# Kernel optimization log

Hardware: AMD Instinct MI355X
Metric: run time of the kernel (lower is better)

Reference implementation:

```python
import jax, jax.numpy as jnp
import numpy as np

EPS = 1e-10
LN_EPS = 1e-5
NEG = -1e30
H = 8  # attention_head


def _layernorm(x, g, b):
    mu = jnp.mean(x, axis=-1, keepdims=True)
    var = jnp.mean(jnp.square(x - mu), axis=-1, keepdims=True)
    return (x - mu) * jax.lax.rsqrt(var + LN_EPS) * g + b


def setup_inputs() -> dict:
    key = jax.random.key(0)
    ks = jax.random.split(key, 10)
    B, T, D = 4, 1024, 1024
    inputs = jax.random.normal(ks[0], (B, T, D), dtype=jnp.float32)
    lengths = jax.random.randint(ks[1], (B,), T // 2, T + 1).astype(jnp.int32)
    lengths = lengths.at[0].set(T)  # at least one full-length sequence
    noise_u = jax.random.uniform(ks[2], (B, H, T, T), dtype=jnp.float32)
    w = lambda k: (jax.random.normal(k, (D, D), dtype=jnp.float32) * 0.02)
    return {
        'inputs': inputs, 'lengths': lengths, 'noise_u': noise_u,
        'Wq': w(ks[3]), 'Wk': w(ks[4]), 'Wv': w(ks[5]),
        'Weq': w(ks[6]), 'Wek': w(ks[7]), 'Wfc': w(ks[8]),
        'bfc': jnp.zeros((D,), jnp.float32),
        'ln1_g': jnp.ones((D,), jnp.float32), 'ln1_b': jnp.zeros((D,), jnp.float32),
        'ln2_g': jnp.ones((D,), jnp.float32), 'ln2_b': jnp.zeros((D,), jnp.float32),
    }


def reference(inputs, lengths, noise_u, Wq, Wk, Wv, Weq, Wek, Wfc, bfc,
              ln1_g, ln1_b, ln2_g, ln2_b):
    B, T, D = inputs.shape
    dh = D // H
    # length mask: True where padded
    pad = jnp.arange(T)[None, :] >= lengths[:, None]            # (B, T)
    x = jnp.where(pad[:, :, None], 0.0, inputs)                  # zero padded positions

    def heads(W):
        h = x @ W.T                                              # (B,T,D)
        return h.reshape(B, T, H, dh).transpose(0, 2, 1, 3)      # (B,H,T,dh)

    q, k, v, eq, ek = (heads(W) for W in (Wq, Wk, Wv, Weq, Wek))
    scores = jnp.einsum('bhqd,bhkd->bhqk', q, k) / jnp.sqrt(jnp.float32(D))
    edge = jnp.einsum('bhqd,bhkd->bhqk', eq, ek)                 # (B,H,T,T)

    # bernoulli prior: binary-concrete sample (hard threshold), tau=1
    edges_prob = jax.nn.sigmoid(edge)
    logistic = jnp.log(noise_u + EPS) - jnp.log(1.0 - noise_u + EPS)
    y_soft = jax.nn.sigmoid(jnp.log(edges_prob + EPS) - jnp.log(1.0 - edges_prob + EPS) + logistic)
    gate = y_soft > 0.5                                          # hard edges (condition only, as in torch .data)

    valid = gate & (~pad[:, None, None, :])                      # gate AND key-length mask
    s = jnp.where(valid, scores, NEG)
    attn = jax.nn.softmax(s, axis=-1)
    attn = jnp.where(jnp.any(valid, axis=-1, keepdims=True), attn, 0.0)  # nan->0 for fully-masked rows

    ctx = jax.nn.relu(jnp.einsum('bhqk,bhkd->bhqd', attn, v))
    ctx = ctx.transpose(0, 2, 1, 3).reshape(B, T, D)

    h1 = _layernorm(ctx + x, ln1_g, ln1_b)
    h2 = jax.nn.relu(h1 @ Wfc.T + bfc) + h1
    out = _layernorm(h2, ln2_g, ln2_b)
    out = jnp.where(pad[:, :, None], 0.0, out)
    return out, attn, edges_prob
```

## Files before the change

### kernel.cpp

```cpp
#include <hip/hip_runtime.h>
#include <math.h>

constexpr int Bn = 4, Tn = 1024, Dn = 1024, Hn = 8, DH = 128;
constexpr float EPSF = 1e-10f;
constexpr float LN_EPSF = 1e-5f;
constexpr float NEGF = -1e30f;

typedef __attribute__((ext_vector_type(8))) short bf16x8;
typedef __attribute__((ext_vector_type(4))) float f32x4;
typedef __attribute__((ext_vector_type(4))) unsigned uint4v;

#define MFMA16(a, b, c) __builtin_amdgcn_mfma_f32_16x16x32_bf16(a, b, c, 0, 0, 0)

__device__ __forceinline__ short f2bf(float f) {
    unsigned u = __builtin_bit_cast(unsigned, f);
    u += 0x7fffu + ((u >> 16) & 1u);
    return (short)(u >> 16);
}
__device__ __forceinline__ float bf2f(short h) {
    return __builtin_bit_cast(float, ((unsigned)(unsigned short)h) << 16);
}
__device__ __forceinline__ unsigned pack2(float a, float b) {
    return ((unsigned)(unsigned short)f2bf(a)) | (((unsigned)(unsigned short)f2bf(b)) << 16);
}

__device__ __forceinline__ void gload16(const void* g, void* l) {
    __builtin_amdgcn_global_load_lds((__attribute__((address_space(1))) void*)g,
                                     (__attribute__((address_space(3))) void*)l,
                                     16, 0, 0);
}

template <int NW>
__device__ __forceinline__ void stage_b(const short* g, int ld, short* lds, int lane, int wid) {
#pragma unroll
    for (int s = 0; s < 8 / NW; ++s) {
        const int ii = wid * (8 / NW) + s;
        const int c = ii * 64 + lane;
        const int kb = c >> 7, r = c & 127;
        gload16(g + (size_t)r * ld + kb * 8, lds + ii * 512);
    }
}

template <int NT>
__device__ __forceinline__ void stage64(const short* g, int ld, short* lds, int lane, int wid) {
    constexpr int IT = 1024 / NT;
#pragma unroll
    for (int s = 0; s < IT; ++s) {
        const int cb = wid * IT + s;
        const int c = cb * 64 + lane;
        const int kb = c >> 7, r = c & 127;
        gload16(g + (size_t)r * ld + kb * 8, lds + cb * 512);
    }
}

template <int NW>
__device__ __forceinline__ void stage_f(const float* g, int ld, float* lds, int lane, int wid) {
#pragma unroll
    for (int s = 0; s < 16 / NW; ++s) {
        const int ii = wid * (16 / NW) + s;
        const int c = ii * 64 + lane;
        const int kb = c >> 8, half = (c >> 7) & 1, r = c & 127;
        gload16(g + (size_t)r * ld + kb * 8 + half * 4, lds + ii * 256);
    }
}

__device__ __forceinline__ bf16x8 fragb(const short* lds, int kbl, int r) {
    return *reinterpret_cast<const bf16x8*>(lds + kbl * 1024 + r * 8);
}

__device__ __forceinline__ bf16x8 fragf(const float* lds, int kbl, int r) {
    const f32x4 lo = *reinterpret_cast<const f32x4*>(lds + kbl * 1024 + r * 4);
    const f32x4 hi = *reinterpret_cast<const f32x4*>(lds + kbl * 1024 + 512 + r * 4);
    uint4v p;
    p[0] = pack2(lo[0], lo[1]);
    p[1] = pack2(lo[2], lo[3]);
    p[2] = pack2(hi[0], hi[1]);
    p[3] = pack2(hi[2], hi[3]);
    return __builtin_bit_cast(bf16x8, p);
}

struct CvtP { const float* src[6]; short* hi; short* lo; };

__global__ __launch_bounds__(256) void cvt_w(CvtP p) {
    const int i = blockIdx.x * 256 + threadIdx.x;
    const int mat = i >> 17;
    const int off = (i & 131071) * 8;
    const float* s = p.src[mat] + off;
    const float4 a = *reinterpret_cast<const float4*>(s);
    const float4 b = *reinterpret_cast<const float4*>(s + 4);
    const float va[8] = {a.x, a.y, a.z, a.w, b.x, b.y, b.z, b.w};
    bf16x8 h, l;
#pragma unroll
    for (int j = 0; j < 8; ++j) {
        h[j] = f2bf(va[j]);
        l[j] = f2bf(va[j] - bf2f(h[j]));
    }
    *reinterpret_cast<bf16x8*>(p.hi + (size_t)mat * 1048576 + off) = h;
    if (mat >= 3)
        *reinterpret_cast<bf16x8*>(p.lo + (size_t)(mat - 3) * 1048576 + off) = l;
}

__global__ __launch_bounds__(256) void mask_x(const float4* __restrict__ in,
                                              const int* __restrict__ lengths,
                                              short* __restrict__ xhi,
                                              short* __restrict__ xlo) {
    const int i = blockIdx.x * 256 + threadIdx.x;
    const int row = i >> 8;
    const int t = row & 1023, b = row >> 10;
    float4 v = in[i];
    if (t >= lengths[b]) { v.x = 0.f; v.y = 0.f; v.z = 0.f; v.w = 0.f; }
    short4 h, l;
    h.x = f2bf(v.x); h.y = f2bf(v.y); h.z = f2bf(v.z); h.w = f2bf(v.w);
    l.x = f2bf(v.x - bf2f(h.x)); l.y = f2bf(v.y - bf2f(h.y));
    l.z = f2bf(v.z - bf2f(h.z)); l.w = f2bf(v.w - bf2f(h.w));
    *reinterpret_cast<short4*>(xhi + (size_t)i * 4) = h;
    *reinterpret_cast<short4*>(xlo + (size_t)i * 4) = l;
}

struct Proj3P { const short* w[3]; short* o[3]; };

__global__ __launch_bounds__(256) void proj3_mfma(const short* __restrict__ Xh, Proj3P p) {
    __shared__ alignas(16) short T0[8192];
    __shared__ alignas(16) short T1[8192];
    const int z = blockIdx.z;
    const short* __restrict__ Wh = p.w[z];
    const int m0 = blockIdx.y << 7, n0 = blockIdx.x << 7;
    const int tid = threadIdx.x, lane = tid & 63, wid = tid >> 6;
    const int wm = (wid >> 1) << 6, wn = (wid & 1) << 6;
    const int kbl = lane >> 4, rl = lane & 15, rw = (lane >> 4) << 2;
    f32x4 acc[4][4] = {};
    for (int k0 = 0; k0 < Dn; k0 += 64) {
        stage64<256>(Xh + (size_t)m0 * Dn + k0, Dn, T0, lane, wid);
        stage64<256>(Wh + (size_t)n0 * Dn + k0, Dn, T1, lane, wid);
        __syncthreads();
#pragma unroll
        for (int hh = 0; hh < 2; ++hh) {
            bf16x8 a[4], b[4];
#pragma unroll
            for (int f = 0; f < 4; ++f) {
                a[f] = fragb(T0, hh * 4 + kbl, wm + f * 16 + rl);
                b[f] = fragb(T1, hh * 4 + kbl, wn + f * 16 + rl);
            }
#pragma unroll
            for (int i = 0; i < 4; ++i)
#pragma unroll
                for (int j = 0; j < 4; ++j)
                    acc[i][j] = MFMA16(a[i], b[j], acc[i][j]);
        }
        __syncthreads();
    }
    short* __restrict__ O = p.o[z];
#pragma unroll
    for (int i = 0; i < 4; ++i)
#pragma unroll
        for (int r = 0; r < 4; ++r) {
            const int m = m0 + wm + i * 16 + rw + r;
            const int b = m >> 10, t = m & 1023;
#pragma unroll
            for (int j = 0; j < 4; ++j) {
                const int n = n0 + wn + j * 16 + rl;
                const int h = n >> 7, d = n & 127;
                const short val = f2bf(acc[i][j][r]);
                if (z == 2)
                    O[(((size_t)(b * Hn + h) * DH + d) << 10) + t] = val;
                else
                    O[((((size_t)(b * Hn + h)) << 10) + t) * DH + d] = val;
            }
        }
}

struct Proj2P { const short* wh[2]; const short* wl[2]; short* oh[2]; short* ol[2]; };

__global__ __launch_bounds__(512) void proj2_mfma(const short* __restrict__ Xh,
                                                  const short* __restrict__ Xl, Proj2P p) {
    __shared__ alignas(16) short T0[8192];
    __shared__ alignas(16) short T1[8192];
    __shared__ alignas(16) short T2[8192];
    __shared__ alignas(16) short T3[8192];
    const int z = blockIdx.z;
    const short* __restrict__ Wh = p.wh[z];
    const short* __restrict__ Wl = p.wl[z];
    const int m0 = blockIdx.y << 7, n0 = blockIdx.x << 7;
    const int tid = threadIdx.x, lane = tid & 63, wid = tid >> 6;
    const int wm = (wid >> 2) << 6, wn = (wid & 3) << 5;
    const int kbl = lane >> 4, rl = lane & 15, rw = (lane >> 4) << 2;
    f32x4 acc[4][2] = {};
    for (int k0 = 0; k0 < Dn; k0 += 64) {
        stage64<512>(Xh + (size_t)m0 * Dn + k0, Dn, T0, lane, wid);
        stage64<512>(Xl + (size_t)m0 * Dn + k0, Dn, T1, lane, wid);
        stage64<512>(Wh + (size_t)n0 * Dn + k0, Dn, T2, lane, wid);
        stage64<512>(Wl + (size_t)n0 * Dn + k0, Dn, T3, lane, wid);
        __syncthreads();
#pragma unroll
        for (int hh = 0; hh < 2; ++hh) {
            bf16x8 ah[4], al[4], bh[2], bl[2];
#pragma unroll
            for (int f = 0; f < 4; ++f) {
                ah[f] = fragb(T0, hh * 4 + kbl, wm + f * 16 + rl);
                al[f] = fragb(T1, hh * 4 + kbl, wm + f * 16 + rl);
            }
#pragma unroll
            for (int f = 0; f < 2; ++f) {
                bh[f] = fragb(T2, hh * 4 + kbl, wn + f * 16 + rl);
                bl[f] = fragb(T3, hh * 4 + kbl, wn + f * 16 + rl);
            }
#pragma unroll
            for (int i = 0; i < 4; ++i)
#pragma unroll
                for (int j = 0; j < 2; ++j) {
                    acc[i][j] = MFMA16(al[i], bh[j], acc[i][j]);
                    acc[i][j] = MFMA16(ah[i], bl[j], acc[i][j]);
                    acc[i][j] = MFMA16(ah[i], bh[j], acc[i][j]);
                }
        }
        __syncthreads();
    }
    short* __restrict__ OH = p.oh[z];
    short* __restrict__ OL = p.ol[z];
#pragma unroll
    for (int i = 0; i < 4; ++i)
#pragma unroll
        for (int r = 0; r < 4; ++r) {
            const int m = m0 + wm + i * 16 + rw + r;
            const int b = m >> 10, t = m & 1023;
#pragma unroll
            for (int j = 0; j < 2; ++j) {
                const int n = n0 + wn + j * 16 + rl;
                const int h = n >> 7, d = n & 127;
                const size_t idx = (((size_t)(b * Hn + h)) << 10 | t) * DH + d;
                const float av = acc[i][j][r];
                const short hi = f2bf(av);
                OH[idx] = hi;
                OL[idx] = f2bf(av - bf2f(hi));
            }
        }
}

__global__ __launch_bounds__(256) void scores_edge(
    const short* __restrict__ Q, const short* __restrict__ Kb,
    const short* __restrict__ EQh, const short* __restrict__ EQl,
    const short* __restrict__ EKh, const short* __restrict__ EKl,
    const float* __restrict__ U, const int* __restrict__ lens,
    float* __restrict__ S, float* __restrict__ EP) {
    __shared__ alignas(16) short T0[4096];
    __shared__ alignas(16) short T1[4096];
    __shared__ alignas(16) short T2[4096];
    __shared__ alignas(16) short T3[4096];
    const int z = blockIdx.z;
    const int len = lens[z >> 3];
    const int m0 = blockIdx.y << 7, n0 = blockIdx.x << 7;
    const int tid = threadIdx.x, lane = tid & 63, wid = tid >> 6;
    const int wm = (wid >> 1) << 6, wn = (wid & 1) << 6;
    const int kbl = lane >> 4, rl = lane & 15, rw = (lane >> 4) << 2;
    const size_t zo = (size_t)z << 17;

    f32x4 acce[4][4] = {};
    for (int k0 = 0; k0 < DH; k0 += 32) {
        stage_b<4>(EQh + zo + (size_t)m0 * DH + k0, DH, T0, lane, wid);
        stage_b<4>(EQl + zo + (size_t)m0 * DH + k0, DH, T1, lane, wid);
        stage_b<4>(EKh + zo + (size_t)n0 * DH + k0, DH, T2, lane, wid);
        stage_b<4>(EKl + zo + (size_t)n0 * DH + k0, DH, T3, lane, wid);
        __syncthreads();
        bf16x8 ah[4], al[4], bh[4], bl[4];
#pragma unroll
        for (int f = 0; f < 4; ++f) {
            ah[f] = fragb(T0, kbl, wm + f * 16 + rl);
            al[f] = fragb(T1, kbl, wm + f * 16 + rl);
            bh[f] = fragb(T2, kbl, wn + f * 16 + rl);
            bl[f] = fragb(T3, kbl, wn + f * 16 + rl);
        }
#pragma unroll
        for (int i = 0; i < 4; ++i)
#pragma unroll
            for (int j = 0; j < 4; ++j) {
                acce[i][j] = MFMA16(al[i], bh[j], acce[i][j]);
                acce[i][j] = MFMA16(ah[i], bl[j], acce[i][j]);
                acce[i][j] = MFMA16(ah[i], bh[j], acce[i][j]);
            }
        __syncthreads();
    }

    f32x4 accs[4][4] = {};
    for (int k0 = 0; k0 < DH; k0 += 32) {
        stage_b<4>(Q + zo + (size_t)m0 * DH + k0, DH, T0, lane, wid);
        stage_b<4>(Kb + zo + (size_t)n0 * DH + k0, DH, T1, lane, wid);
        __syncthreads();
        bf16x8 a[4], b[4];
#pragma unroll
        for (int f = 0; f < 4; ++f) {
            a[f] = fragb(T0, kbl, wm + f * 16 + rl);
            b[f] = fragb(T1, kbl, wn + f * 16 + rl);
        }
#pragma unroll
        for (int i = 0; i < 4; ++i)
#pragma unroll
            for (int j = 0; j < 4; ++j)
                accs[i][j] = MFMA16(a[i], b[j], accs[i][j]);
        __syncthreads();
    }

#pragma unroll
    for (int i = 0; i < 4; ++i)
#pragma unroll
        for (int r = 0; r < 4; ++r) {
            const int m = m0 + wm + i * 16 + rw + r;
#pragma unroll
            for (int j = 0; j < 4; ++j) {
                const int n = n0 + wn + j * 16 + rl;
                const size_t idx = ((size_t)z << 20) + ((size_t)m << 10) + n;
                const float e = acce[i][j][r];
                EP[idx] = 1.f / (1.f + __expf(-e));
                const float u = U[idx];
                const float zz = e + __logf(u + EPSF) - __logf(1.f - u + EPSF);
                const bool valid = (zz > 0.f) && (n < len);
                S[idx] = valid ? accs[i][j][r] * (1.f / 32.f) : NEGF;
            }
        }
}

__global__ __launch_bounds__(512) void softmax_ctx(float* __restrict__ P,
                                                   const short* __restrict__ Vt,
                                                   float* __restrict__ C) {
    __shared__ alignas(16) float Ps[4096];
    __shared__ alignas(16) short Vs[4096];
    const int z = blockIdx.y;
    const int bb = z >> 3, h = z & 7;
    const int m0 = blockIdx.x << 7;
    const int tid = threadIdx.x, lane = tid & 63, wid = tid >> 6;

    {
        const int r = tid >> 2, qd = tid & 3;
        float* rowp = P + ((size_t)z << 20) + ((size_t)(m0 + r) << 10) + qd * 8;
        float mrun = -3.0e38f, lrun = 0.f;
#pragma unroll 8
        for (int c = 0; c < 32; ++c) {
            const float4 v0 = *reinterpret_cast<const float4*>(rowp + c * 32);
            const float4 v1 = *reinterpret_cast<const float4*>(rowp + c * 32 + 4);
            const float cm = fmaxf(fmaxf(fmaxf(v0.x, v0.y), fmaxf(v0.z, v0.w)),
                                   fmaxf(fmaxf(v1.x, v1.y), fmaxf(v1.z, v1.w)));
            const float mn = fmaxf(mrun, cm);
            lrun = lrun * __expf(mrun - mn) +
                   __expf(v0.x - mn) + __expf(v0.y - mn) +
                   __expf(v0.z - mn) + __expf(v0.w - mn) +
                   __expf(v1.x - mn) + __expf(v1.y - mn) +
                   __expf(v1.z - mn) + __expf(v1.w - mn);
            mrun = mn;
        }
#pragma unroll
        for (int off = 1; off <= 2; off <<= 1) {
            const float mo = __shfl_xor(mrun, off);
            const float lo2 = __shfl_xor(lrun, off);
            const float mn = fmaxf(mrun, mo);
            lrun = lrun * __expf(mrun - mn) + lo2 * __expf(mo - mn);
            mrun = mn;
        }
        const float inv = (mrun > -5e29f) ? 1.f / lrun : 0.f;
#pragma unroll 8
        for (int c = 0; c < 32; ++c) {
            float4 v0 = *reinterpret_cast<const float4*>(rowp + c * 32);
            float4 v1 = *reinterpret_cast<const float4*>(rowp + c * 32 + 4);
            v0.x = __expf(v0.x - mrun) * inv; v0.y = __expf(v0.y - mrun) * inv;
            v0.z = __expf(v0.z - mrun) * inv; v0.w = __expf(v0.w - mrun) * inv;
            v1.x = __expf(v1.x - mrun) * inv; v1.y = __expf(v1.y - mrun) * inv;
            v1.z = __expf(v1.z - mrun) * inv; v1.w = __expf(v1.w - mrun) * inv;
            *reinterpret_cast<float4*>(rowp + c * 32) = v0;
            *reinterpret_cast<float4*>(rowp + c * 32 + 4) = v1;
        }
    }
    __syncthreads();

    const int wm = (wid >> 2) << 6, wn = (wid & 3) << 5;
    const int kbl = lane >> 4, rl = lane & 15, rw = (lane >> 4) << 2;
    f32x4 acc[4][2] = {};
    for (int k0 = 0; k0 < Tn; k0 += 32) {
        stage_f<8>(P + ((size_t)z << 20) + ((size_t)m0 << 10) + k0, Tn, Ps, lane, wid);
        stage_b<8>(Vt + ((size_t)z << 17) + k0, Tn, Vs, lane, wid);
        __syncthreads();
        bf16x8 a[4], b[2];
#pragma unroll
        for (int f = 0; f < 4; ++f) a[f] = fragf(Ps, kbl, wm + f * 16 + rl);
#pragma unroll
        for (int f = 0; f < 2; ++f) b[f] = fragb(Vs, kbl, wn + f * 16 + rl);
#pragma unroll
        for (int i = 0; i < 4; ++i)
#pragma unroll
            for (int j = 0; j < 2; ++j)
                acc[i][j] = MFMA16(a[i], b[j], acc[i][j]);
        __syncthreads();
    }
#pragma unroll
    for (int i = 0; i < 4; ++i)
#pragma unroll
        for (int r = 0; r < 4; ++r) {
            const int m = m0 + wm + i * 16 + rw + r;
#pragma unroll
            for (int j = 0; j < 2; ++j) {
                const int n = wn + j * 16 + rl;
                C[(((size_t)(bb << 10 | m)) << 10) + h * DH + n] = fmaxf(acc[i][j][r], 0.f);
            }
        }
}

__global__ __launch_bounds__(256) void ln1_kernel(const float* __restrict__ ctx,
                                                  const float* __restrict__ inputs,
                                                  const int* __restrict__ lengths,
                                                  const float* __restrict__ g,
                                                  const float* __restrict__ bb,
                                                  float* __restrict__ h1f,
                                                  short* __restrict__ h1hi,
                                                  short* __restrict__ h1lo) {
    __shared__ float red1[4];
    __shared__ float red2[4];
    const int row = blockIdx.x;
    const int t = row & 1023, b = row >> 10;
    const bool live = t < lengths[b];
    const size_t base = (size_t)row * Dn;
    const int tid = threadIdx.x;
    float4 v = reinterpret_cast<const float4*>(ctx + base)[tid];
    if (live) {
        const float4 r = reinterpret_cast<const float4*>(inputs + base)[tid];
        v.x += r.x; v.y += r.y; v.z += r.z; v.w += r.w;
    }
    float s = v.x + v.y + v.z + v.w;
#pragma unroll
    for (int off = 32; off >= 1; off >>= 1) s += __shfl_xor(s, off);
    if ((tid & 63) == 0) red1[tid >> 6] = s;
    __syncthreads();
    const float mu = (red1[0] + red1[1] + red1[2] + red1[3]) * (1.f / Dn);
    const float d0 = v.x - mu, d1 = v.y - mu, d2 = v.z - mu, d3 = v.w - mu;
    float sq = d0 * d0 + d1 * d1 + d2 * d2 + d3 * d3;
#pragma unroll
    for (int off = 32; off >= 1; off >>= 1) sq += __shfl_xor(sq, off);
    if ((tid & 63) == 0) red2[tid >> 6] = sq;
    __syncthreads();
    const float var = (red2[0] + red2[1] + red2[2] + red2[3]) * (1.f / Dn);
    const float rstd = rsqrtf(var + LN_EPSF);
    const float4 gv = reinterpret_cast<const float4*>(g)[tid];
    const float4 bv = reinterpret_cast<const float4*>(bb)[tid];
    float4 ov;
    ov.x = d0 * rstd * gv.x + bv.x;
    ov.y = d1 * rstd * gv.y + bv.y;
    ov.z = d2 * rstd * gv.z + bv.z;
    ov.w = d3 * rstd * gv.w + bv.w;
    reinterpret_cast<float4*>(h1f + base)[tid] = ov;
    short4 hs, ls;
    hs.x = f2bf(ov.x); hs.y = f2bf(ov.y); hs.z = f2bf(ov.z); hs.w = f2bf(ov.w);
    ls.x = f2bf(ov.x - bf2f(hs.x)); ls.y = f2bf(ov.y - bf2f(hs.y));
    ls.z = f2bf(ov.z - bf2f(hs.z)); ls.w = f2bf(ov.w - bf2f(hs.w));
    reinterpret_cast<short4*>(h1hi + base)[tid] = hs;
    reinterpret_cast<short4*>(h1lo + base)[tid] = ls;
}

__global__ __launch_bounds__(512) void fc_mfma(const short* __restrict__ Xh,
                                               const short* __restrict__ Xl,
                                               const short* __restrict__ Wh,
                                               const short* __restrict__ Wl,
                                               const float* __restrict__ bias,
                                               const float* __restrict__ H1f,
                                               float* __restrict__ O) {
    __shared__ alignas(16) short T0[8192];
    __shared__ alignas(16) short T1[8192];
    __shared__ alignas(16) short T2[8192];
    __shared__ alignas(16) short T3[8192];
    const int m0 = blockIdx.y << 7, n0 = blockIdx.x << 7;
    const int tid = threadIdx.x, lane = tid & 63, wid = tid >> 6;
    const int wm = (wid >> 2) << 6, wn = (wid & 3) << 5;
    const int kbl = lane >> 4, rl = lane & 15, rw = (lane >> 4) << 2;
    f32x4 acc[4][2] = {};
    for (int k0 = 0; k0 < Dn; k0 += 64) {
        stage64<512>(Xh + (size_t)m0 * Dn + k0, Dn, T0, lane, wid);
        stage64<512>(Xl + (size_t)m0 * Dn + k0, Dn, T1, lane, wid);
        stage64<512>(Wh + (size_t)n0 * Dn + k0, Dn, T2, lane, wid);
        stage64<512>(Wl + (size_t)n0 * Dn + k0, Dn, T3, lane, wid);
        __syncthreads();
#pragma unroll
        for (int hh = 0; hh < 2; ++hh) {
            bf16x8 ah[4], al[4], bh[2], bl[2];
#pragma unroll
            for (int f = 0; f < 4; ++f) {
                ah[f] = fragb(T0, hh * 4 + kbl, wm + f * 16 + rl);
                al[f] = fragb(T1, hh * 4 + kbl, wm + f * 16 + rl);
            }
#pragma unroll
            for (int f = 0; f < 2; ++f) {
                bh[f] = fragb(T2, hh * 4 + kbl, wn + f * 16 + rl);
                bl[f] = fragb(T3, hh * 4 + kbl, wn + f * 16 + rl);
            }
#pragma unroll
            for (int i = 0; i < 4; ++i)
#pragma unroll
                for (int j = 0; j < 2; ++j) {
                    acc[i][j] = MFMA16(al[i], bh[j], acc[i][j]);
                    acc[i][j] = MFMA16(ah[i], bl[j], acc[i][j]);
                    acc[i][j] = MFMA16(ah[i], bh[j], acc[i][j]);
                }
        }
        __syncthreads();
    }
#pragma unroll
    for (int i = 0; i < 4; ++i)
#pragma unroll
        for (int r = 0; r < 4; ++r) {
            const int m = m0 + wm + i * 16 + rw + r;
#pragma unroll
            for (int j = 0; j < 2; ++j) {
                const int n = n0 + wn + j * 16 + rl;
                const size_t idx = ((size_t)m << 10) + n;
                O[idx] = fmaxf(acc[i][j][r] + bias[n], 0.f) + H1f[idx];
            }
        }
}

__global__ __launch_bounds__(256) void ln2_kernel(const float* __restrict__ a,
                                                  const float* __restrict__ g,
                                                  const float* __restrict__ bb,
                                                  const int* __restrict__ lengths,
                                                  float* __restrict__ o) {
    __shared__ float red1[4];
    __shared__ float red2[4];
    const int row = blockIdx.x;
    const size_t base = (size_t)row * Dn;
    const int tid = threadIdx.x;
    float4 v = reinterpret_cast<const float4*>(a + base)[tid];
    float s = v.x + v.y + v.z + v.w;
#pragma unroll
    for (int off = 32; off >= 1; off >>= 1) s += __shfl_xor(s, off);
    if ((tid & 63) == 0) red1[tid >> 6] = s;
    __syncthreads();
    const float mu = (red1[0] + red1[1] + red1[2] + red1[3]) * (1.f / Dn);
    const float d0 = v.x - mu, d1 = v.y - mu, d2 = v.z - mu, d3 = v.w - mu;
    float sq = d0 * d0 + d1 * d1 + d2 * d2 + d3 * d3;
#pragma unroll
    for (int off = 32; off >= 1; off >>= 1) sq += __shfl_xor(sq, off);
    if ((tid & 63) == 0) red2[tid >> 6] = sq;
    __syncthreads();
    const float var = (red2[0] + red2[1] + red2[2] + red2[3]) * (1.f / Dn);
    const float rstd = rsqrtf(var + LN_EPSF);
    const float4 gv = reinterpret_cast<const float4*>(g)[tid];
    const float4 bv = reinterpret_cast<const float4*>(bb)[tid];
    float4 ov;
    ov.x = d0 * rstd * gv.x + bv.x;
    ov.y = d1 * rstd * gv.y + bv.y;
    ov.z = d2 * rstd * gv.z + bv.z;
    ov.w = d3 * rstd * gv.w + bv.w;
    const int t = row & 1023, b = row >> 10;
    if (t >= lengths[b]) { ov.x = 0.f; ov.y = 0.f; ov.z = 0.f; ov.w = 0.f; }
    reinterpret_cast<float4*>(o + base)[tid] = ov;
}

extern "C" void kernel_launch(void* const* d_in, const int* in_sizes, int n_in,
                              void* d_out, int out_size, void* d_ws, size_t ws_size,
                              hipStream_t stream) {
    const float* inputs = (const float*)d_in[0];
    const int* lengths = (const int*)d_in[1];
    const float* noise = (const float*)d_in[2];
    const float* bfc = (const float*)d_in[9];
    const float* ln1_g = (const float*)d_in[10];
    const float* ln1_b = (const float*)d_in[11];
    const float* ln2_g = (const float*)d_in[12];
    const float* ln2_b = (const float*)d_in[13];

    float* out = (float*)d_out;
    float* attn = out + (size_t)Bn * Tn * Dn;
    float* ep = attn + (size_t)Bn * Hn * Tn * Tn;

    constexpr size_t MB = 1u << 20;
    char* W = (char*)d_ws;
    short* xhi = (short*)(W + 0 * MB);
    short* xlo = (short*)(W + 8 * MB);
    short* whi = (short*)(W + 16 * MB);
    short* wlo = (short*)(W + 28 * MB);
    short* qb = (short*)(W + 34 * MB);
    short* kb = (short*)(W + 42 * MB);
    short* vtb = (short*)(W + 50 * MB);
    short* eqh = (short*)(W + 58 * MB);
    short* eql = (short*)(W + 66 * MB);
    short* ekh = (short*)(W + 74 * MB);
    short* ekl = (short*)(W + 82 * MB);
    float* ctx = (float*)(W + 58 * MB);
    float* h1f = (float*)(W + 74 * MB);
    short* h1hi = (short*)(W + 34 * MB);
    short* h1lo = (short*)(W + 42 * MB);
    float* h2 = (float*)(W + 0 * MB);

    CvtP cp;
    for (int j = 0; j < 6; ++j) cp.src[j] = (const float*)d_in[3 + j];
    cp.hi = whi; cp.lo = wlo;
    cvt_w<<<dim3(3072), 256, 0, stream>>>(cp);

    mask_x<<<dim3(4096), 256, 0, stream>>>((const float4*)inputs, lengths, xhi, xlo);

    Proj3P p3;
    p3.w[0] = whi;                 p3.o[0] = qb;
    p3.w[1] = whi + 1 * 1048576;   p3.o[1] = kb;
    p3.w[2] = whi + 2 * 1048576;   p3.o[2] = vtb;
    proj3_mfma<<<dim3(8, 32, 3), 256, 0, stream>>>(xhi, p3);

    Proj2P p2;
    p2.wh[0] = whi + 3 * 1048576;  p2.wl[0] = wlo;
    p2.wh[1] = whi + 4 * 1048576;  p2.wl[1] = wlo + 1048576;
    p2.oh[0] = eqh; p2.ol[0] = eql;
    p2.oh[1] = ekh; p2.ol[1] = ekl;
    proj2_mfma<<<dim3(8, 32, 2), 512, 0, stream>>>(xhi, xlo, p2);

    scores_edge<<<dim3(8, 8, 32), 256, 0, stream>>>(qb, kb, eqh, eql, ekh, ekl,
                                                    noise, lengths, attn, ep);

    softmax_ctx<<<dim3(8, 32), 512, 0, stream>>>(attn, vtb, ctx);

    ln1_kernel<<<dim3(Bn * Tn), 256, 0, stream>>>(ctx, inputs, lengths, ln1_g, ln1_b,
                                                  h1f, h1hi, h1lo);

    fc_mfma<<<dim3(8, 32), 512, 0, stream>>>(h1hi, h1lo, whi + 5 * 1048576,
                                             wlo + 2 * 1048576, bfc, h1f, h2);

    ln2_kernel<<<dim3(Bn * Tn), 256, 0, stream>>>(h2, ln2_g, ln2_b, lengths, out);
}
```

Baseline: 516.3 us.

## Fuse softmax row statistics into scores epilogue and drop split-bf16 in FC

The scores kernel now computes per-row partial max and sum-of-exp for each 64-column warp slice and writes them to workspace. The softmax kernel merges these partials, so it no longer makes a separate read pass over the 128MB score matrix. Separately, the FC GEMM drops the hi/lo split-bf16 compensation and runs a single bf16 MFMA per tile with a 256-thread layout, and LN1 no longer writes the low part. This cuts a full read of the attention matrix and two-thirds of the FC MFMAs, at the cost of lower FC precision.

```diff
diff --git a/kernel.cpp b/kernel.cpp
--- a/kernel.cpp
+++ b/kernel.cpp
@@ -96,7 +96,7 @@
         l[j] = f2bf(va[j] - bf2f(h[j]));
     }
     *reinterpret_cast<bf16x8*>(p.hi + (size_t)mat * 1048576 + off) = h;
-    if (mat >= 3)
+    if (mat == 3 || mat == 4)
         *reinterpret_cast<bf16x8*>(p.lo + (size_t)(mat - 3) * 1048576 + off) = l;
 }
 
@@ -241,7 +241,8 @@
     const short* __restrict__ EQh, const short* __restrict__ EQl,
     const short* __restrict__ EKh, const short* __restrict__ EKl,
     const float* __restrict__ U, const int* __restrict__ lens,
-    float* __restrict__ S, float* __restrict__ EP) {
+    float* __restrict__ S, float* __restrict__ EP,
+    float* __restrict__ Sm, float* __restrict__ Sl) {
     __shared__ alignas(16) short T0[4096];
     __shared__ alignas(16) short T1[4096];
     __shared__ alignas(16) short T2[4096];
@@ -299,11 +300,13 @@
         __syncthreads();
     }
 
+    const size_t part = ((size_t)(z * 16 + blockIdx.x * 2 + (wn >> 6)) << 10);
 #pragma unroll
     for (int i = 0; i < 4; ++i)
 #pragma unroll
         for (int r = 0; r < 4; ++r) {
             const int m = m0 + wm + i * 16 + rw + r;
+            float sv[4];
 #pragma unroll
             for (int j = 0; j < 4; ++j) {
                 const int n = n0 + wn + j * 16 + rl;
@@ -313,12 +316,24 @@
                 const float u = U[idx];
                 const float zz = e + __logf(u + EPSF) - __logf(1.f - u + EPSF);
                 const bool valid = (zz > 0.f) && (n < len);
-                S[idx] = valid ? accs[i][j][r] * (1.f / 32.f) : NEGF;
-            }
+                const float s_val = valid ? accs[i][j][r] * (1.f / 32.f) : NEGF;
+                S[idx] = s_val;
+                sv[j] = s_val;
+            }
+            float mx = fmaxf(fmaxf(sv[0], sv[1]), fmaxf(sv[2], sv[3]));
+#pragma unroll
+            for (int off = 1; off <= 8; off <<= 1) mx = fmaxf(mx, __shfl_xor(mx, off));
+            float ls = __expf(sv[0] - mx) + __expf(sv[1] - mx) +
+                       __expf(sv[2] - mx) + __expf(sv[3] - mx);
+#pragma unroll
+            for (int off = 1; off <= 8; off <<= 1) ls += __shfl_xor(ls, off);
+            if (rl == 0) { Sm[part + m] = mx; Sl[part + m] = ls; }
         }
 }
 
 __global__ __launch_bounds__(512) void softmax_ctx(float* __restrict__ P,
+                                                   const float* __restrict__ Sm,
+                                                   const float* __restrict__ Sl,
                                                    const short* __restrict__ Vt,
                                                    float* __restrict__ C) {
     __shared__ alignas(16) float Ps[4096];
@@ -330,39 +345,25 @@
 
     {
         const int r = tid >> 2, qd = tid & 3;
-        float* rowp = P + ((size_t)z << 20) + ((size_t)(m0 + r) << 10) + qd * 8;
-        float mrun = -3.0e38f, lrun = 0.f;
-#pragma unroll 8
-        for (int c = 0; c < 32; ++c) {
-            const float4 v0 = *reinterpret_cast<const float4*>(rowp + c * 32);
-            const float4 v1 = *reinterpret_cast<const float4*>(rowp + c * 32 + 4);
-            const float cm = fmaxf(fmaxf(fmaxf(v0.x, v0.y), fmaxf(v0.z, v0.w)),
-                                   fmaxf(fmaxf(v1.x, v1.y), fmaxf(v1.z, v1.w)));
-            const float mn = fmaxf(mrun, cm);
-            lrun = lrun * __expf(mrun - mn) +
-                   __expf(v0.x - mn) + __expf(v0.y - mn) +
-                   __expf(v0.z - mn) + __expf(v0.w - mn) +
-                   __expf(v1.x - mn) + __expf(v1.y - mn) +
-                   __expf(v1.z - mn) + __expf(v1.w - mn);
-            mrun = mn;
-        }
-#pragma unroll
-        for (int off = 1; off <= 2; off <<= 1) {
-            const float mo = __shfl_xor(mrun, off);
-            const float lo2 = __shfl_xor(lrun, off);
-            const float mn = fmaxf(mrun, mo);
-            lrun = lrun * __expf(mrun - mn) + lo2 * __expf(mo - mn);
-            mrun = mn;
-        }
-        const float inv = (mrun > -5e29f) ? 1.f / lrun : 0.f;
+        const int row = m0 + r;
+        float M = -3.0e38f;
+#pragma unroll
+        for (int t = 0; t < 16; ++t) M = fmaxf(M, Sm[((size_t)(z * 16 + t) << 10) + row]);
+        float L = 0.f;
+#pragma unroll
+        for (int t = 0; t < 16; ++t)
+            L += Sl[((size_t)(z * 16 + t) << 10) + row] *
+                 __expf(Sm[((size_t)(z * 16 + t) << 10) + row] - M);
+        const float inv = (M > -5e29f) ? 1.f / L : 0.f;
+        float* rowp = P + ((size_t)z << 20) + ((size_t)row << 10) + qd * 8;
 #pragma unroll 8
         for (int c = 0; c < 32; ++c) {
             float4 v0 = *reinterpret_cast<const float4*>(rowp + c * 32);
             float4 v1 = *reinterpret_cast<const float4*>(rowp + c * 32 + 4);
-            v0.x = __expf(v0.x - mrun) * inv; v0.y = __expf(v0.y - mrun) * inv;
-            v0.z = __expf(v0.z - mrun) * inv; v0.w = __expf(v0.w - mrun) * inv;
-            v1.x = __expf(v1.x - mrun) * inv; v1.y = __expf(v1.y - mrun) * inv;
-            v1.z = __expf(v1.z - mrun) * inv; v1.w = __expf(v1.w - mrun) * inv;
+            v0.x = __expf(v0.x - M) * inv; v0.y = __expf(v0.y - M) * inv;
+            v0.z = __expf(v0.z - M) * inv; v0.w = __expf(v0.w - M) * inv;
+            v1.x = __expf(v1.x - M) * inv; v1.y = __expf(v1.y - M) * inv;
+            v1.z = __expf(v1.z - M) * inv; v1.w = __expf(v1.w - M) * inv;
             *reinterpret_cast<float4*>(rowp + c * 32) = v0;
             *reinterpret_cast<float4*>(rowp + c * 32 + 4) = v1;
         }
@@ -407,8 +408,7 @@
                                                   const float* __restrict__ g,
                                                   const float* __restrict__ bb,
                                                   float* __restrict__ h1f,
-                                                  short* __restrict__ h1hi,
-                                                  short* __restrict__ h1lo) {
+                                                  short* __restrict__ h1hi) {
     __shared__ float red1[4];
     __shared__ float red2[4];
     const int row = blockIdx.x;
@@ -443,57 +443,40 @@
     ov.z = d2 * rstd * gv.z + bv.z;
     ov.w = d3 * rstd * gv.w + bv.w;
     reinterpret_cast<float4*>(h1f + base)[tid] = ov;
-    short4 hs, ls;
+    short4 hs;
     hs.x = f2bf(ov.x); hs.y = f2bf(ov.y); hs.z = f2bf(ov.z); hs.w = f2bf(ov.w);
-    ls.x = f2bf(ov.x - bf2f(hs.x)); ls.y = f2bf(ov.y - bf2f(hs.y));
-    ls.z = f2bf(ov.z - bf2f(hs.z)); ls.w = f2bf(ov.w - bf2f(hs.w));
     reinterpret_cast<short4*>(h1hi + base)[tid] = hs;
-    reinterpret_cast<short4*>(h1lo + base)[tid] = ls;
-}
-
-__global__ __launch_bounds__(512) void fc_mfma(const short* __restrict__ Xh,
-                                               const short* __restrict__ Xl,
+}
+
+__global__ __launch_bounds__(256) void fc_mfma(const short* __restrict__ Xh,
                                                const short* __restrict__ Wh,
-                                               const short* __restrict__ Wl,
                                                const float* __restrict__ bias,
                                                const float* __restrict__ H1f,
                                                float* __restrict__ O) {
     __shared__ alignas(16) short T0[8192];
     __shared__ alignas(16) short T1[8192];
-    __shared__ alignas(16) short T2[8192];
-    __shared__ alignas(16) short T3[8192];
     const int m0 = blockIdx.y << 7, n0 = blockIdx.x << 7;
     const int tid = threadIdx.x, lane = tid & 63, wid = tid >> 6;
-    const int wm = (wid >> 2) << 6, wn = (wid & 3) << 5;
+    const int wm = (wid >> 1) << 6, wn = (wid & 1) << 6;
     const int kbl = lane >> 4, rl = lane & 15, rw = (lane >> 4) << 2;
-    f32x4 acc[4][2] = {};
+    f32x4 acc[4][4] = {};
     for (int k0 = 0; k0 < Dn; k0 += 64) {
-        stage64<512>(Xh + (size_t)m0 * Dn + k0, Dn, T0, lane, wid);
-        stage64<512>(Xl + (size_t)m0 * Dn + k0, Dn, T1, lane, wid);
-        stage64<512>(Wh + (size_t)n0 * Dn + k0, Dn, T2, lane, wid);
-        stage64<512>(Wl + (size_t)n0 * Dn + k0, Dn, T3, lane, wid);
+        stage64<256>(Xh + (size_t)m0 * Dn + k0, Dn, T0, lane, wid);
+        stage64<256>(Wh + (size_t)n0 * Dn + k0, Dn, T1, lane, wid);
         __syncthreads();
 #pragma unroll
         for (int hh = 0; hh < 2; ++hh) {
-            bf16x8 ah[4], al[4], bh[2], bl[2];
+            bf16x8 a[4], b[4];
 #pragma unroll
             for (int f = 0; f < 4; ++f) {
-                ah[f] = fragb(T0, hh * 4 + kbl, wm + f * 16 + rl);
-                al[f] = fragb(T1, hh * 4 + kbl, wm + f * 16 + rl);
-            }
-#pragma unroll
-            for (int f = 0; f < 2; ++f) {
-                bh[f] = fragb(T2, hh * 4 + kbl, wn + f * 16 + rl);
-                bl[f] = fragb(T3, hh * 4 + kbl, wn + f * 16 + rl);
+                a[f] = fragb(T0, hh * 4 + kbl, wm + f * 16 + rl);
+                b[f] = fragb(T1, hh * 4 + kbl, wn + f * 16 + rl);
             }
 #pragma unroll
             for (int i = 0; i < 4; ++i)
 #pragma unroll
-                for (int j = 0; j < 2; ++j) {
-                    acc[i][j] = MFMA16(al[i], bh[j], acc[i][j]);
-                    acc[i][j] = MFMA16(ah[i], bl[j], acc[i][j]);
-                    acc[i][j] = MFMA16(ah[i], bh[j], acc[i][j]);
-                }
+                for (int j = 0; j < 4; ++j)
+                    acc[i][j] = MFMA16(a[i], b[j], acc[i][j]);
         }
         __syncthreads();
     }
@@ -503,7 +486,7 @@
         for (int r = 0; r < 4; ++r) {
             const int m = m0 + wm + i * 16 + rw + r;
 #pragma unroll
-            for (int j = 0; j < 2; ++j) {
+            for (int j = 0; j < 4; ++j) {
                 const int n = n0 + wn + j * 16 + rl;
                 const size_t idx = ((size_t)m << 10) + n;
                 O[idx] = fmaxf(acc[i][j][r] + bias[n], 0.f) + H1f[idx];
@@ -580,8 +563,9 @@
     float* ctx = (float*)(W + 58 * MB);
     float* h1f = (float*)(W + 74 * MB);
     short* h1hi = (short*)(W + 34 * MB);
-    short* h1lo = (short*)(W + 42 * MB);
     float* h2 = (float*)(W + 0 * MB);
+    float* Sm = (float*)(W + 90 * MB);
+    float* Sl = (float*)(W + 92 * MB);
 
     CvtP cp;
     for (int j = 0; j < 6; ++j) cp.src[j] = (const float*)d_in[3 + j];
@@ -604,15 +588,14 @@
     proj2_mfma<<<dim3(8, 32, 2), 512, 0, stream>>>(xhi, xlo, p2);
 
     scores_edge<<<dim3(8, 8, 32), 256, 0, stream>>>(qb, kb, eqh, eql, ekh, ekl,
-                                                    noise, lengths, attn, ep);
-
-    softmax_ctx<<<dim3(8, 32), 512, 0, stream>>>(attn, vtb, ctx);
+                                                    noise, lengths, attn, ep, Sm, Sl);
+
+    softmax_ctx<<<dim3(8, 32), 512, 0, stream>>>(attn, Sm, Sl, vtb, ctx);
 
     ln1_kernel<<<dim3(Bn * Tn), 256, 0, stream>>>(ctx, inputs, lengths, ln1_g, ln1_b,
-                                                  h1f, h1hi, h1lo);
-
-    fc_mfma<<<dim3(8, 32), 512, 0, stream>>>(h1hi, h1lo, whi + 5 * 1048576,
-                                             wlo + 2 * 1048576, bfc, h1f, h2);
+                                                  h1f, h1hi);
+
+    fc_mfma<<<dim3(8, 32), 256, 0, stream>>>(h1hi, whi + 5 * 1048576, bfc, h1f, h2);
 
     ln2_kernel<<<dim3(Bn * Tn), 256, 0, stream>>>(h2, ln2_g, ln2_b, lengths, out);
 }
```

After: 500.2 us. 1.03x faster.
